# Kernel tuning notes

Measured on AMD Instinct MI355X. Metric: run time of the kernel, lower is better.

## Reference

```python
import jax, jax.numpy as jnp
import numpy as np

L_COORD = 5.0
L_NOOBJ = 0.5
NUM_B = 2


def setup_inputs() -> dict:
    key = jax.random.key(0)
    ks = jax.random.split(key, 6)
    N, S, Bb, C = 4096, 14, NUM_B, 20
    pred_cls = jax.random.uniform(ks[0], (N, S, S, C), dtype=jnp.float32)
    pred_response = jax.random.uniform(ks[1], (N, S, S, Bb), dtype=jnp.float32)
    pred_bboxes = jax.random.uniform(ks[2], (N, S, S, Bb * 4), dtype=jnp.float32)
    label_cls = jax.random.uniform(ks[3], (N, S, S, C), dtype=jnp.float32)
    # binary objectness per cell, tiled over the B response channels
    obj_bit = jax.random.randint(ks[4], (N, S, S), 0, 2).astype(jnp.float32)
    label_response = jnp.tile(obj_bit[..., None], (1, 1, 1, Bb))
    label_bboxes = jax.random.uniform(ks[5], (N, S, S, Bb * 4), dtype=jnp.float32)
    return {
        "pred_cls": pred_cls,
        "pred_response": pred_response,
        "pred_bboxes": pred_bboxes,
        "label_cls": label_cls,
        "label_response": label_response,
        "label_bboxes": label_bboxes,
    }


def _to_corners(p):
    # p: [..., B, 4] with (x, y, sqrt_w, sqrt_h); corners via w = sqrt_w**2
    xy = p[..., 0:2]
    half_wh = 0.5 * p[..., 2:4] ** 2
    return jnp.concatenate([xy - half_wh, xy + half_wh], axis=-1)


def _iou_elementwise(b1, b2):
    # b1, b2: [..., 4] corner boxes; elementwise IoU (matches compute_iou with N==M broadcast)
    lt = jnp.maximum(b1[..., 0:2], b2[..., 0:2])
    rb = jnp.minimum(b1[..., 2:4], b2[..., 2:4])
    wh = jnp.maximum(rb - lt, 0.0)
    inter = wh[..., 0] * wh[..., 1]
    a1 = (b1[..., 2] - b1[..., 0]) * (b1[..., 3] - b1[..., 1])
    a2 = (b2[..., 2] - b2[..., 0]) * (b2[..., 3] - b2[..., 1])
    return inter / (a1 + a2 - inter)


def reference(pred_cls, pred_response, pred_bboxes, label_cls, label_response, label_bboxes):
    N, S = pred_response.shape[0], pred_response.shape[1]
    Bb = NUM_B
    bs = jnp.float32(N)

    obj = (label_response[..., 0] > 0).astype(pred_cls.dtype)      # [N,S,S]
    noobj = (label_response[..., 0] < 1).astype(pred_cls.dtype)    # [N,S,S]

    # no-object containment loss over all B channels
    nobj_loss = jnp.sum(noobj[..., None] * (pred_response - label_response) ** 2) / bs

    # class loss on object cells
    cls_loss = jnp.sum(obj[..., None] * (pred_cls - label_cls) ** 2) / bs

    # per-box IoU between matching pred/target boxes j (dense, masked later)
    pb = pred_bboxes.reshape(N, S, S, Bb, 4)
    tb = label_bboxes.reshape(N, S, S, Bb, 4)
    iou = _iou_elementwise(_to_corners(tb), _to_corners(pb))  # [N,S,S,B]

    max_iou = jnp.max(iou, axis=-1)                            # [N,S,S]
    best = jnp.argmax(iou, axis=-1)                            # [N,S,S]

    best_p = jnp.take_along_axis(pb, best[..., None, None], axis=3)[:, :, :, 0, :]  # [N,S,S,4]
    best_t = jnp.take_along_axis(tb, best[..., None, None], axis=3)[:, :, :, 0, :]
    pred_resp_best = jnp.take_along_axis(pred_response, best[..., None], axis=-1)[..., 0]
    label_resp_best = jnp.take_along_axis(label_response, best[..., None], axis=-1)[..., 0]

    # coordinate loss on the responsible box (xy + sqrt-wh terms)
    coord_loss = jnp.sum(obj[..., None] * (best_p - best_t) ** 2) / bs

    # max_iou is detached in the original (.data)
    max_iou_d = jax.lax.stop_gradient(max_iou)
    pobj_loss = jnp.sum(obj * (pred_resp_best - max_iou_d) ** 2) / bs
    iou_loss = jnp.sum(obj * (max_iou_d - label_resp_best) ** 2) / bs

    # [offset, cls, pObj, nObj, iou]
    return jnp.stack([L_COORD * coord_loss, cls_loss, pobj_loss, L_NOOBJ * nobj_loss, iou_loss])
```

## Files before the change

### kernel.cpp

```cpp
#include <hip/hip_runtime.h>


constexpr int NCELL    = 4096 * 14 * 14;
constexpr int TPB      = 256;
constexpr int BLOCKS   = NCELL / TPB;
constexpr int NTHREADS = NCELL;
constexpr int CLS_IT   = 5;
constexpr int BOX_IT   = 2;

constexpr float INV_BS  = 1.0f / 4096.0f;
constexpr float L_COORD = 5.0f;
constexpr float L_NOOBJ = 0.5f;

__device__ __forceinline__ float iou_corners(float4 t, float4 p) {
    float thx = 0.5f * t.z * t.z;
    float thy = 0.5f * t.w * t.w;
    float t_l = t.x - thx, t_t = t.y - thy;
    float t_r = t.x + thx, t_b = t.y + thy;
    float phx = 0.5f * p.z * p.z;
    float phy = 0.5f * p.w * p.w;
    float p_l = p.x - phx, p_t = p.y - phy;
    float p_r = p.x + phx, p_b = p.y + phy;
    float ltx = fmaxf(t_l, p_l), lty = fmaxf(t_t, p_t);
    float rbx = fminf(t_r, p_r), rby = fminf(t_b, p_b);
    float wx = fmaxf(rbx - ltx, 0.0f), wy = fmaxf(rby - lty, 0.0f);
    float inter = wx * wy;
    float a1 = (t_r - t_l) * (t_b - t_t);
    float a2 = (p_r - p_l) * (p_b - p_t);
    return inter / (a1 + a2 - inter);
}

__global__ __launch_bounds__(TPB) void yolo_loss_main(
    const float* __restrict__ pred_cls,
    const float* __restrict__ pred_resp,
    const float* __restrict__ pred_bb,
    const float* __restrict__ label_cls,
    const float* __restrict__ label_resp,
    const float* __restrict__ label_bb,
    float* __restrict__ ws)
{
    const int tid = blockIdx.x * TPB + threadIdx.x;

    float coord = 0.0f, cls = 0.0f, pobj = 0.0f, nobj = 0.0f, iouL = 0.0f;

    const float4* pc4 = reinterpret_cast<const float4*>(pred_cls);
    const float4* lc4 = reinterpret_cast<const float4*>(label_cls);
    #pragma unroll
    for (int j = 0; j < CLS_IT; ++j) {
        unsigned i4 = (unsigned)(j * NTHREADS + tid);
        float4 a = pc4[i4];
        float4 b = lc4[i4];
        unsigned cell = i4 / 5u;
        float o = (label_resp[(size_t)cell * 2] > 0.0f) ? 1.0f : 0.0f;
        float dx = a.x - b.x, dy = a.y - b.y, dz = a.z - b.z, dw = a.w - b.w;
        cls += o * (dx * dx + dy * dy + dz * dz + dw * dw);
    }

    const float4* pb4 = reinterpret_cast<const float4*>(pred_bb);
    const float4* tb4 = reinterpret_cast<const float4*>(label_bb);
    #pragma unroll
    for (int j = 0; j < BOX_IT; ++j) {
        int bi = j * NTHREADS + tid;
        float4 p = pb4[bi];
        float4 t = tb4[bi];
        float prv = pred_resp[bi];
        float lrv = label_resp[bi];

        float iou   = iou_corners(t, p);
        float iou_o = __shfl_xor(iou, 1);
        bool  is_b1 = (bi & 1);
        bool  win   = is_b1 ? (iou > iou_o) : (iou >= iou_o);
        float mx    = fmaxf(iou, iou_o);

        float obj = (lrv > 0.0f) ? 1.0f : 0.0f;
        float dr  = prv - lrv;
        nobj += (1.0f - obj) * dr * dr;

        float wm = win ? obj : 0.0f;
        float ex = p.x - t.x, ey = p.y - t.y, ez = p.z - t.z, ew = p.w - t.w;
        coord += wm * (ex * ex + ey * ey + ez * ez + ew * ew);
        float dpo = prv - mx;
        float dio = mx - lrv;
        pobj += wm * dpo * dpo;
        iouL += wm * dio * dio;
    }

    #pragma unroll
    for (int off = 32; off > 0; off >>= 1) {
        coord += __shfl_down(coord, off);
        cls   += __shfl_down(cls,   off);
        pobj  += __shfl_down(pobj,  off);
        nobj  += __shfl_down(nobj,  off);
        iouL  += __shfl_down(iouL,  off);
    }

    __shared__ float part[4][5];
    int wave = threadIdx.x >> 6;
    int lane = threadIdx.x & 63;
    if (lane == 0) {
        part[wave][0] = coord;
        part[wave][1] = cls;
        part[wave][2] = pobj;
        part[wave][3] = nobj;
        part[wave][4] = iouL;
    }
    __syncthreads();
    if (threadIdx.x == 0) {
        float* w = ws + (size_t)blockIdx.x * 8;
        w[0] = part[0][0] + part[1][0] + part[2][0] + part[3][0];
        w[1] = part[0][1] + part[1][1] + part[2][1] + part[3][1];
        w[2] = part[0][2] + part[1][2] + part[2][2] + part[3][2];
        w[3] = part[0][3] + part[1][3] + part[2][3] + part[3][3];
        w[4] = part[0][4] + part[1][4] + part[2][4] + part[3][4];
    }
}

__global__ __launch_bounds__(TPB) void yolo_loss_finish(
    const float* __restrict__ ws,
    float* __restrict__ out)
{
    float s0 = 0.0f, s1 = 0.0f, s2 = 0.0f, s3 = 0.0f, s4 = 0.0f;
    for (int b = threadIdx.x; b < BLOCKS; b += TPB) {
        const float* w = ws + (size_t)b * 8;
        s0 += w[0]; s1 += w[1]; s2 += w[2]; s3 += w[3]; s4 += w[4];
    }
    #pragma unroll
    for (int off = 32; off > 0; off >>= 1) {
        s0 += __shfl_down(s0, off);
        s1 += __shfl_down(s1, off);
        s2 += __shfl_down(s2, off);
        s3 += __shfl_down(s3, off);
        s4 += __shfl_down(s4, off);
    }
    __shared__ float part[4][5];
    int wave = threadIdx.x >> 6;
    int lane = threadIdx.x & 63;
    if (lane == 0) {
        part[wave][0] = s0; part[wave][1] = s1; part[wave][2] = s2;
        part[wave][3] = s3; part[wave][4] = s4;
    }
    __syncthreads();
    if (threadIdx.x == 0) {
        float t0 = part[0][0] + part[1][0] + part[2][0] + part[3][0];
        float t1 = part[0][1] + part[1][1] + part[2][1] + part[3][1];
        float t2 = part[0][2] + part[1][2] + part[2][2] + part[3][2];
        float t3 = part[0][3] + part[1][3] + part[2][3] + part[3][3];
        float t4 = part[0][4] + part[1][4] + part[2][4] + part[3][4];
        out[0] = L_COORD * INV_BS * t0;
        out[1] = INV_BS * t1;
        out[2] = INV_BS * t2;
        out[3] = L_NOOBJ * INV_BS * t3;
        out[4] = INV_BS * t4;
    }
}

extern "C" void kernel_launch(void* const* d_in, const int* in_sizes, int n_in,
                              void* d_out, int out_size, void* d_ws, size_t ws_size,
                              hipStream_t stream) {
    const float* pred_cls   = (const float*)d_in[0];
    const float* pred_resp  = (const float*)d_in[1];
    const float* pred_bb    = (const float*)d_in[2];
    const float* label_cls  = (const float*)d_in[3];
    const float* label_resp = (const float*)d_in[4];
    const float* label_bb   = (const float*)d_in[5];
    float* ws  = (float*)d_ws;
    float* out = (float*)d_out;

    yolo_loss_main<<<BLOCKS, TPB, 0, stream>>>(
        pred_cls, pred_resp, pred_bb, label_cls, label_resp, label_bb, ws);
    yolo_loss_finish<<<1, TPB, 0, stream>>>(ws, out);
}
```

Measured before the change: 203.0 us.

## Process whole cells per thread and skip loading class/box data for empty cells

Each thread now handles two full grid cells instead of striding over flattened float4 slices. It reads the objectness label first and only fetches class and box data for object cells. Non-object cells are redirected to cell 0's address, which should be served from cache. This removes most DRAM reads for roughly half the cells and drops the cross-lane shuffle for the IoU argmax. The cost is a less regular per-thread access pattern (80-byte and 32-byte contiguous chunks per thread) and dependent loads that wait on the objectness read.

```diff
diff --git a/kernel.cpp b/kernel.cpp
--- a/kernel.cpp
+++ b/kernel.cpp
@@ -1,12 +1,11 @@
 #include <hip/hip_runtime.h>
 
 
-constexpr int NCELL    = 4096 * 14 * 14;
-constexpr int TPB      = 256;
-constexpr int BLOCKS   = NCELL / TPB;
-constexpr int NTHREADS = NCELL;
-constexpr int CLS_IT   = 5;
-constexpr int BOX_IT   = 2;
+constexpr int NCELL  = 4096 * 14 * 14;
+constexpr int TPB    = 256;
+constexpr int CPT    = 2;
+constexpr int BLOCKS = NCELL / (TPB * CPT);
+constexpr int NT     = BLOCKS * TPB;
 
 constexpr float INV_BS  = 1.0f / 4096.0f;
 constexpr float L_COORD = 5.0f;
@@ -30,7 +29,7 @@
     return inter / (a1 + a2 - inter);
 }
 
-__global__ __launch_bounds__(TPB) void yolo_loss_main(
+__global__ __launch_bounds__(TPB, 1) void yolo_loss_main(
     const float* __restrict__ pred_cls,
     const float* __restrict__ pred_resp,
     const float* __restrict__ pred_bb,
@@ -39,50 +38,98 @@
     const float* __restrict__ label_bb,
     float* __restrict__ ws)
 {
-    const int tid = blockIdx.x * TPB + threadIdx.x;
-
-    float coord = 0.0f, cls = 0.0f, pobj = 0.0f, nobj = 0.0f, iouL = 0.0f;
+    const int tid   = blockIdx.x * TPB + threadIdx.x;
+    const int cellA = tid;
+    const int cellB = tid + NT;
 
     const float4* pc4 = reinterpret_cast<const float4*>(pred_cls);
     const float4* lc4 = reinterpret_cast<const float4*>(label_cls);
-    #pragma unroll
-    for (int j = 0; j < CLS_IT; ++j) {
-        unsigned i4 = (unsigned)(j * NTHREADS + tid);
-        float4 a = pc4[i4];
-        float4 b = lc4[i4];
-        unsigned cell = i4 / 5u;
-        float o = (label_resp[(size_t)cell * 2] > 0.0f) ? 1.0f : 0.0f;
-        float dx = a.x - b.x, dy = a.y - b.y, dz = a.z - b.z, dw = a.w - b.w;
-        cls += o * (dx * dx + dy * dy + dz * dz + dw * dw);
-    }
-
     const float4* pb4 = reinterpret_cast<const float4*>(pred_bb);
     const float4* tb4 = reinterpret_cast<const float4*>(label_bb);
-    #pragma unroll
-    for (int j = 0; j < BOX_IT; ++j) {
-        int bi = j * NTHREADS + tid;
-        float4 p = pb4[bi];
-        float4 t = tb4[bi];
-        float prv = pred_resp[bi];
-        float lrv = label_resp[bi];
-
-        float iou   = iou_corners(t, p);
-        float iou_o = __shfl_xor(iou, 1);
-        bool  is_b1 = (bi & 1);
-        bool  win   = is_b1 ? (iou > iou_o) : (iou >= iou_o);
-        float mx    = fmaxf(iou, iou_o);
-
-        float obj = (lrv > 0.0f) ? 1.0f : 0.0f;
-        float dr  = prv - lrv;
-        nobj += (1.0f - obj) * dr * dr;
-
-        float wm = win ? obj : 0.0f;
-        float ex = p.x - t.x, ey = p.y - t.y, ez = p.z - t.z, ew = p.w - t.w;
-        coord += wm * (ex * ex + ey * ey + ez * ez + ew * ew);
-        float dpo = prv - mx;
-        float dio = mx - lrv;
-        pobj += wm * dpo * dpo;
-        iouL += wm * dio * dio;
+
+    float2 lrA = *reinterpret_cast<const float2*>(label_resp + (size_t)cellA * 2);
+    float2 prA = *reinterpret_cast<const float2*>(pred_resp  + (size_t)cellA * 2);
+    float2 lrB = *reinterpret_cast<const float2*>(label_resp + (size_t)cellB * 2);
+    float2 prB = *reinterpret_cast<const float2*>(pred_resp  + (size_t)cellB * 2);
+
+    const float objA = (lrA.x > 0.0f) ? 1.0f : 0.0f;
+    const float objB = (lrB.x > 0.0f) ? 1.0f : 0.0f;
+
+    const size_t baA = (lrA.x > 0.0f) ? (size_t)cellA : 0;
+    const size_t baB = (lrB.x > 0.0f) ? (size_t)cellB : 0;
+
+    float4 A0 = pc4[baA * 5 + 0], A1 = pc4[baA * 5 + 1], A2 = pc4[baA * 5 + 2],
+           A3 = pc4[baA * 5 + 3], A4 = pc4[baA * 5 + 4];
+    float4 La0 = lc4[baA * 5 + 0], La1 = lc4[baA * 5 + 1], La2 = lc4[baA * 5 + 2],
+           La3 = lc4[baA * 5 + 3], La4 = lc4[baA * 5 + 4];
+    float4 pbA0 = pb4[baA * 2 + 0], pbA1 = pb4[baA * 2 + 1];
+    float4 tbA0 = tb4[baA * 2 + 0], tbA1 = tb4[baA * 2 + 1];
+
+    float4 B0 = pc4[baB * 5 + 0], B1 = pc4[baB * 5 + 1], B2 = pc4[baB * 5 + 2],
+           B3 = pc4[baB * 5 + 3], B4 = pc4[baB * 5 + 4];
+    float4 Lb0 = lc4[baB * 5 + 0], Lb1 = lc4[baB * 5 + 1], Lb2 = lc4[baB * 5 + 2],
+           Lb3 = lc4[baB * 5 + 3], Lb4 = lc4[baB * 5 + 4];
+    float4 pbB0 = pb4[baB * 2 + 0], pbB1 = pb4[baB * 2 + 1];
+    float4 tbB0 = tb4[baB * 2 + 0], tbB1 = tb4[baB * 2 + 1];
+
+    float coord = 0.0f, cls = 0.0f, pobj = 0.0f, nobj = 0.0f, iouL = 0.0f;
+
+    {
+        float d0 = prA.x - lrA.x, d1 = prA.y - lrA.y;
+        nobj += (1.0f - objA) * (d0 * d0 + d1 * d1);
+
+        float c = 0.0f, dx, dy, dz, dw;
+        dx = A0.x-La0.x; dy = A0.y-La0.y; dz = A0.z-La0.z; dw = A0.w-La0.w; c += dx*dx+dy*dy+dz*dz+dw*dw;
+        dx = A1.x-La1.x; dy = A1.y-La1.y; dz = A1.z-La1.z; dw = A1.w-La1.w; c += dx*dx+dy*dy+dz*dz+dw*dw;
+        dx = A2.x-La2.x; dy = A2.y-La2.y; dz = A2.z-La2.z; dw = A2.w-La2.w; c += dx*dx+dy*dy+dz*dz+dw*dw;
+        dx = A3.x-La3.x; dy = A3.y-La3.y; dz = A3.z-La3.z; dw = A3.w-La3.w; c += dx*dx+dy*dy+dz*dz+dw*dw;
+        dx = A4.x-La4.x; dy = A4.y-La4.y; dz = A4.z-La4.z; dw = A4.w-La4.w; c += dx*dx+dy*dy+dz*dz+dw*dw;
+        cls += objA * c;
+
+        float iou0 = iou_corners(tbA0, pbA0);
+        float iou1 = iou_corners(tbA1, pbA1);
+        bool  best1 = iou1 > iou0;
+        float mx = fmaxf(iou0, iou1);
+
+        float4 bp = best1 ? pbA1 : pbA0;
+        float4 bt = best1 ? tbA1 : tbA0;
+        float ex = bp.x - bt.x, ey = bp.y - bt.y, ez = bp.z - bt.z, ew = bp.w - bt.w;
+        coord += objA * (ex * ex + ey * ey + ez * ez + ew * ew);
+
+        float pr_b = best1 ? prA.y : prA.x;
+        float lr_b = best1 ? lrA.y : lrA.x;
+        float dpo = pr_b - mx, dio = mx - lr_b;
+        pobj += objA * dpo * dpo;
+        iouL += objA * dio * dio;
+    }
+
+    {
+        float d0 = prB.x - lrB.x, d1 = prB.y - lrB.y;
+        nobj += (1.0f - objB) * (d0 * d0 + d1 * d1);
+
+        float c = 0.0f, dx, dy, dz, dw;
+        dx = B0.x-Lb0.x; dy = B0.y-Lb0.y; dz = B0.z-Lb0.z; dw = B0.w-Lb0.w; c += dx*dx+dy*dy+dz*dz+dw*dw;
+        dx = B1.x-Lb1.x; dy = B1.y-Lb1.y; dz = B1.z-Lb1.z; dw = B1.w-Lb1.w; c += dx*dx+dy*dy+dz*dz+dw*dw;
+        dx = B2.x-Lb2.x; dy = B2.y-Lb2.y; dz = B2.z-Lb2.z; dw = B2.w-Lb2.w; c += dx*dx+dy*dy+dz*dz+dw*dw;
+        dx = B3.x-Lb3.x; dy = B3.y-Lb3.y; dz = B3.z-Lb3.z; dw = B3.w-Lb3.w; c += dx*dx+dy*dy+dz*dz+dw*dw;
+        dx = B4.x-Lb4.x; dy = B4.y-Lb4.y; dz = B4.z-Lb4.z; dw = B4.w-Lb4.w; c += dx*dx+dy*dy+dz*dz+dw*dw;
+        cls += objB * c;
+
+        float iou0 = iou_corners(tbB0, pbB0);
+        float iou1 = iou_corners(tbB1, pbB1);
+        bool  best1 = iou1 > iou0;
+        float mx = fmaxf(iou0, iou1);
+
+        float4 bp = best1 ? pbB1 : pbB0;
+        float4 bt = best1 ? tbB1 : tbB0;
+        float ex = bp.x - bt.x, ey = bp.y - bt.y, ez = bp.z - bt.z, ew = bp.w - bt.w;
+        coord += objB * (ex * ex + ey * ey + ez * ez + ew * ew);
+
+        float pr_b = best1 ? prB.y : prB.x;
+        float lr_b = best1 ? lrB.y : lrB.x;
+        float dpo = pr_b - mx, dio = mx - lr_b;
+        pobj += objB * dpo * dpo;
+        iouL += objB * dio * dio;
     }
 
     #pragma unroll
```

Result: faster. 197.9 us (-2.5%).

## Skip loads for non-object cells and switch to grid-stride loops

Applied to the files above, without the earlier changes.

For cells whose label response is zero, the box and class loads are redirected to element 0, so memory traffic is skipped for cells whose contribution is masked out anyway. The kernel also moves from one fixed-work thread per cell to a grid-stride loop over 2048 blocks, with the box pass first and the class pass second. This cuts DRAM reads in a memory-bound kernel. Savings depend on the objectness pattern and on cache-line granularity, and the redirected loads add a dependency on the label_resp load before the big loads can issue.

```diff
diff --git a/kernel.cpp b/kernel.cpp
--- a/kernel.cpp
+++ b/kernel.cpp
@@ -1,12 +1,12 @@
 #include <hip/hip_runtime.h>
 
 
-constexpr int NCELL    = 4096 * 14 * 14;
-constexpr int TPB      = 256;
-constexpr int BLOCKS   = NCELL / TPB;
-constexpr int NTHREADS = NCELL;
-constexpr int CLS_IT   = 5;
-constexpr int BOX_IT   = 2;
+constexpr int NCELL  = 4096 * 14 * 14;
+constexpr int TPB    = 256;
+constexpr int BLOCKS = 2048;
+constexpr int NT     = BLOCKS * TPB;
+constexpr int N4CLS  = NCELL * 5;
+constexpr int NBOX   = NCELL * 2;
 
 constexpr float INV_BS  = 1.0f / 4096.0f;
 constexpr float L_COORD = 5.0f;
@@ -39,32 +39,24 @@
     const float* __restrict__ label_bb,
     float* __restrict__ ws)
 {
-    const int tid = blockIdx.x * TPB + threadIdx.x;
+    const int gtid = blockIdx.x * TPB + threadIdx.x;
+
+    const float4* pc4 = reinterpret_cast<const float4*>(pred_cls);
+    const float4* lc4 = reinterpret_cast<const float4*>(label_cls);
+    const float4* pb4 = reinterpret_cast<const float4*>(pred_bb);
+    const float4* tb4 = reinterpret_cast<const float4*>(label_bb);
 
     float coord = 0.0f, cls = 0.0f, pobj = 0.0f, nobj = 0.0f, iouL = 0.0f;
 
-    const float4* pc4 = reinterpret_cast<const float4*>(pred_cls);
-    const float4* lc4 = reinterpret_cast<const float4*>(label_cls);
-    #pragma unroll
-    for (int j = 0; j < CLS_IT; ++j) {
-        unsigned i4 = (unsigned)(j * NTHREADS + tid);
-        float4 a = pc4[i4];
-        float4 b = lc4[i4];
-        unsigned cell = i4 / 5u;
-        float o = (label_resp[(size_t)cell * 2] > 0.0f) ? 1.0f : 0.0f;
-        float dx = a.x - b.x, dy = a.y - b.y, dz = a.z - b.z, dw = a.w - b.w;
-        cls += o * (dx * dx + dy * dy + dz * dz + dw * dw);
-    }
+    #pragma unroll 2
+    for (int bi = gtid; bi < NBOX; bi += NT) {
+        float lrv = label_resp[bi];
+        float prv = pred_resp[bi];
+        bool  objb = lrv > 0.0f;
+        int   be   = objb ? bi : 0;
 
-    const float4* pb4 = reinterpret_cast<const float4*>(pred_bb);
-    const float4* tb4 = reinterpret_cast<const float4*>(label_bb);
-    #pragma unroll
-    for (int j = 0; j < BOX_IT; ++j) {
-        int bi = j * NTHREADS + tid;
-        float4 p = pb4[bi];
-        float4 t = tb4[bi];
-        float prv = pred_resp[bi];
-        float lrv = label_resp[bi];
+        float4 p = pb4[be];
+        float4 t = tb4[be];
 
         float iou   = iou_corners(t, p);
         float iou_o = __shfl_xor(iou, 1);
@@ -72,17 +64,31 @@
         bool  win   = is_b1 ? (iou > iou_o) : (iou >= iou_o);
         float mx    = fmaxf(iou, iou_o);
 
-        float obj = (lrv > 0.0f) ? 1.0f : 0.0f;
-        float dr  = prv - lrv;
-        nobj += (1.0f - obj) * dr * dr;
+        float o  = objb ? 1.0f : 0.0f;
+        float dr = prv - lrv;
+        nobj += (1.0f - o) * dr * dr;
 
-        float wm = win ? obj : 0.0f;
+        float wm = (win ? 1.0f : 0.0f) * o;
         float ex = p.x - t.x, ey = p.y - t.y, ez = p.z - t.z, ew = p.w - t.w;
         coord += wm * (ex * ex + ey * ey + ez * ez + ew * ew);
         float dpo = prv - mx;
         float dio = mx - lrv;
         pobj += wm * dpo * dpo;
         iouL += wm * dio * dio;
+    }
+
+    #pragma unroll 2
+    for (int i4 = gtid; i4 < N4CLS; i4 += NT) {
+        unsigned cell = (unsigned)i4 / 5u;
+        float m = label_resp[(size_t)cell * 2];
+        bool  objc = m > 0.0f;
+        int   ie   = objc ? i4 : 0;
+
+        float4 a = pc4[ie];
+        float4 b = lc4[ie];
+        float dx = a.x - b.x, dy = a.y - b.y, dz = a.z - b.z, dw = a.w - b.w;
+        float s = dx * dx + dy * dy + dz * dz + dw * dw;
+        cls += (objc ? 1.0f : 0.0f) * s;
     }
 
     #pragma unroll
```

New measurement: 195.0 us. -3.9%, faster.
